# Optimization experiments

Measured on AMD Instinct MI355X. Metric: run time of the kernel, lower is better.

Reference implementation:

```python
import jax, jax.numpy as jnp
import numpy as np


def setup_inputs() -> dict:
    key = jax.random.key(0)
    ks = jax.random.split(key, 6)
    Bsz, Ch, N, L = 16, 1024, 16, 4096
    return {
        "input": jax.random.normal(ks[0], (Bsz, Ch, L), jnp.float32),
        "A": jax.random.normal(ks[1], (Ch, N, 2), jnp.float32),
        "B": jax.random.normal(ks[2], (Ch, N), jnp.float32),  # unused in 'dws' mode
        "C": jax.random.normal(ks[3], (Ch, N), jnp.float32),  # unused in 'dws' mode
        "log_dt": jax.random.normal(ks[4], (Ch, N), jnp.float32) * 0.5 - 4.0,
        "E": jax.random.normal(ks[5], (Ch, N), jnp.float32),
    }


def reference(input, A, B, C, log_dt, E):
    """Kernelizer forward, mode='dws', run_mode='training'.

    discretize (simplified ZOH):
      A_real = -softplus(A[...,0]); A_imag = A[...,1]; dt = exp(log_dt)
      E_hat = E * dt; dtA = dt * (A_real + i*A_imag)        # (Ch, N)
    kernel: k[c, l] = Re( sum_n E_hat[c,n] * exp(dtA[c,n] * l) )
    output: causal depthwise conv of input with k via 2L-padded FFT.
    """
    L = input.shape[-1]
    A_real = -jax.nn.softplus(A[..., 0])                     # (Ch, N)
    A_imag = A[..., 1]                                       # (Ch, N)
    dt = jnp.exp(log_dt)                                     # (Ch, N)
    E_hat = E * dt                                           # (Ch, N)
    dtA_real = dt * A_real
    dtA_imag = dt * A_imag

    l = jnp.arange(L, dtype=input.dtype)                     # (L,)
    # real part of the complex vandermonde, fused: exp(ar*l) * cos(ai*l)
    vand = jnp.exp(dtA_real[:, :, None] * l) * jnp.cos(dtA_imag[:, :, None] * l)  # (Ch, N, L)
    k = jnp.einsum('cn,cnl->cl', E_hat, vand)                # (Ch, L)

    n_fft = 2 * L  # zero-pad so circular conv == linear causal conv
    Uf = jnp.fft.rfft(input, n=n_fft)                        # (B, Ch, L+1)
    Kf = jnp.fft.rfft(k, n=n_fft)                            # (Ch, L+1)
    y = jnp.fft.irfft(Uf * Kf, n=n_fft)[..., :L]             # (B, Ch, L)
    return y.astype(input.dtype)
```

## Files before the change

### kernel.cpp

```cpp
#include <hip/hip_runtime.h>

#define CH   1024
#define BSZ  16
#define LSEQ 4096
#define NST  16

typedef __attribute__((ext_vector_type(8))) short short8;
typedef __attribute__((ext_vector_type(4))) float f32x4;

__device__ __forceinline__ unsigned int pk2(float a, float b) {
    unsigned int ua = __float_as_uint(a);
    unsigned int ub = __float_as_uint(b);
    ua = (ua + 0x7fffu + ((ua >> 16) & 1u)) >> 16;
    ub = (ub + 0x7fffu + ((ub >> 16) & 1u)) & 0xffff0000u;
    return ua | ub;
}

#define P_BYTES 12582912
#define W_BYTES 4194304

__global__ __launch_bounds__(64) void setup_k(const float* __restrict__ A,
                                              const float* __restrict__ log_dt,
                                              const float* __restrict__ E,
                                              unsigned int* __restrict__ Pw,
                                              unsigned int* __restrict__ Ww,
                                              float* __restrict__ qw) {
    __shared__ float powr[NST][65], powi[NST][65], eh[NST], klds[64];
    const int t = threadIdx.x, c = blockIdx.x;
    const int n = t & 15;
    const int idx = c * NST + n;
    float a0 = A[2 * idx], a1 = A[2 * idx + 1];
    float sp = (a0 > 20.f) ? a0 : log1pf(expf(a0));
    float dt = expf(log_dt[idx]);
    float dar = -dt * sp, dai = dt * a1;
    float ehv = E[idx] * dt;
    if (t < NST) eh[t] = ehv;
    for (int l = t >> 4; l < 65; l += 4) {
        float mg = expf(dar * (float)l);
        float s, cs;
        sincosf(dai * (float)l, &s, &cs);
        powr[n][l] = mg * cs;
        powi[n][l] = mg * s;
    }
    __syncthreads();
    float kl = 0.f;
#pragma unroll
    for (int nn = 0; nn < NST; ++nn) kl += eh[nn] * powr[nn][t];
    klds[t] = kl;
    __syncthreads();
    unsigned int* Pc = Pw + c * 3072;
    for (int kk = 0; kk < 48; ++kk) {
        int d = kk * 64 + t;
        int i = d / 48;
        int k0 = (d - i * 48) * 2;
        float vv[2];
#pragma unroll
        for (int u = 0; u < 2; ++u) {
            int k = k0 + u;
            if (k < 64) vv[u] = (k <= i) ? klds[i - k] : 0.f;
            else {
                int p = k - 64;
                int nn = p >> 1;
                vv[u] = (p & 1) ? (-eh[nn] * powi[nn][i + 1]) : (eh[nn] * powr[nn][i + 1]);
            }
        }
        Pc[d] = pk2(vv[0], vv[1]);
    }
    unsigned int* Wc = Ww + c * 1024;
    for (int kk = 0; kk < 16; ++kk) {
        int d = kk * 64 + t;
        int p = d >> 5;
        int j0 = (d & 31) * 2;
        int nn = p >> 1;
        float v0 = (p & 1) ? powi[nn][63 - j0] : powr[nn][63 - j0];
        float v1 = (p & 1) ? powi[nn][62 - j0] : powr[nn][62 - j0];
        Wc[d] = pk2(v0, v1);
    }
    if (t < 32) qw[c * 32 + t] = (t & 1) ? powi[t >> 1][64] : powr[t >> 1][64];
}

#define XT0_OFF 0
#define XT1_OFF 8192
#define S_OFF   16384
#define SIN_OFF 24704
#define SMEM_SZ 28800

__global__ __launch_bounds__(256) void conv_k(const float* __restrict__ x,
                                              const char* __restrict__ Pb,
                                              const char* __restrict__ Wb,
                                              const float* __restrict__ qw,
                                              float* __restrict__ y) {
    __shared__ __align__(16) char smem[SMEM_SZ];
    const int tid  = threadIdx.x;
    const int w    = tid >> 6, lane = tid & 63;
    const int g    = lane >> 4, l15 = lane & 15;
    const int c    = blockIdx.x;

    const char* Pc = Pb + (size_t)c * 12288;
    const char* Wc = Wb + (size_t)c * 4096;
    short8 wa[2], pa[3];
    {
        int p = 16 * (w >> 1) + l15;
#pragma unroll
        for (int kt = 0; kt < 2; ++kt)
            wa[kt] = *(const short8*)(Wc + p * 128 + kt * 64 + g * 16);
        int i = 16 * w + l15;
#pragma unroll
        for (int kt = 0; kt < 3; ++kt)
            pa[kt] = *(const short8*)(Pc + i * 192 + kt * 64 + g * 16);
    }
    float qr0[4], qi0[4];
#pragma unroll
    for (int k = 0; k < 4; ++k) {
        int nn = 4 * w + k;
        qr0[k] = qw[c * 32 + 2 * nn];
        qi0[k] = qw[c * 32 + 2 * nn + 1];
    }

    float* S = (float*)(smem + S_OFF);

    const int st_m    = tid >> 4;
    const int st_base = 8 * (tid & 15);

    auto stage = [&](int xoff, const float4* v) {
#pragma unroll
        for (int it = 0; it < 4; ++it) {
            int m = 16 * it + st_m;
            int byte = (m * 128 + st_base) ^ ((m & 7) << 4);
            *(uint2*)(smem + xoff + byte) =
                make_uint2(pk2(v[it].x, v[it].y), pk2(v[it].z, v[it].w));
        }
    };

    auto gemm1 = [&](int xoff) {
        f32x4 acc[2] = {{0.f, 0.f, 0.f, 0.f}, {0.f, 0.f, 0.f, 0.f}};
        int ntb = 2 * (w & 1);
#pragma unroll
        for (int nt = 0; nt < 2; ++nt) {
            int m = l15 + 16 * (ntb + nt);
            int sw = (m & 7) << 4;
#pragma unroll
            for (int kt = 0; kt < 2; ++kt) {
                short8 bf = *(const short8*)(smem + xoff + ((m * 128 + kt * 64 + g * 16) ^ sw));
                acc[nt] = __builtin_amdgcn_mfma_f32_16x16x32_bf16(wa[kt], bf, acc[nt], 0, 0, 0);
            }
        }
        int pbase = 16 * (w >> 1) + 4 * g;
#pragma unroll
        for (int nt = 0; nt < 2; ++nt) {
            int m = l15 + 16 * (ntb + nt);
#pragma unroll
            for (int r = 0; r < 4; ++r)
                S[(pbase + r) * 65 + m] = acc[nt][r];
        }
    };

    auto scan = [&]() {
        float sr[4], si[4], qr[4], qi[4];
#pragma unroll
        for (int k = 0; k < 4; ++k) {
            int nn = 4 * w + k;
            sr[k] = S[(2 * nn) * 65 + lane];
            si[k] = S[(2 * nn + 1) * 65 + lane];
            qr[k] = qr0[k];
            qi[k] = qi0[k];
        }
#pragma unroll
        for (int d = 1; d < 64; d <<= 1) {
#pragma unroll
            for (int k = 0; k < 4; ++k) {
                float ur = __shfl_up(sr[k], d);
                float ui = __shfl_up(si[k], d);
                ur = (lane >= d) ? ur : 0.f;
                ui = (lane >= d) ? ui : 0.f;
                sr[k] = fmaf(qr[k], ur, fmaf(-qi[k], ui, sr[k]));
                si[k] = fmaf(qr[k], ui, fmaf(qi[k], ur, si[k]));
            }
#pragma unroll
            for (int k = 0; k < 4; ++k) {
                float tq = fmaf(qr[k], qr[k], -(qi[k] * qi[k]));
                qi[k] = 2.f * qr[k] * qi[k];
                qr[k] = tq;
            }
        }
        unsigned int dw[4];
#pragma unroll
        for (int k = 0; k < 4; ++k) {
            float ar = __shfl_up(sr[k], 1);
            float ai = __shfl_up(si[k], 1);
            ar = (lane > 0) ? ar : 0.f;
            ai = (lane > 0) ? ai : 0.f;
            dw[k] = pk2(ar, ai);
        }
        int byte = (lane * 64 + 16 * w) ^ ((lane & 3) << 4);
        *(uint4*)(smem + SIN_OFF + byte) = make_uint4(dw[0], dw[1], dw[2], dw[3]);
    };

    auto gemm2 = [&](int xoff, float* yr) {
        f32x4 acc[4] = {{0.f,0.f,0.f,0.f},{0.f,0.f,0.f,0.f},{0.f,0.f,0.f,0.f},{0.f,0.f,0.f,0.f}};
#pragma unroll
        for (int nt = 0; nt < 4; ++nt) {
            int m = l15 + 16 * nt;
            int sw = (m & 7) << 4;
#pragma unroll
            for (int kt = 0; kt < 2; ++kt) {
                short8 bf = *(const short8*)(smem + xoff + ((m * 128 + kt * 64 + g * 16) ^ sw));
                acc[nt] = __builtin_amdgcn_mfma_f32_16x16x32_bf16(pa[kt], bf, acc[nt], 0, 0, 0);
            }
            short8 sf = *(const short8*)(smem + SIN_OFF + ((m * 64 + g * 16) ^ ((m & 3) << 4)));
            acc[nt] = __builtin_amdgcn_mfma_f32_16x16x32_bf16(pa[2], sf, acc[nt], 0, 0, 0);
        }
#pragma unroll
        for (int nt = 0; nt < 4; ++nt) {
            int m = l15 + 16 * nt;
            float4 v = make_float4(acc[nt][0], acc[nt][1], acc[nt][2], acc[nt][3]);
            *(float4*)(yr + m * 64 + 16 * w + 4 * g) = v;
        }
    };

    const size_t cstride = (size_t)CH * LSEQ;
    const float* xr = x + (size_t)c * LSEQ + 4 * tid;
    float*       yb = y + (size_t)c * LSEQ;

    float4 v[4];
#pragma unroll
    for (int it = 0; it < 4; ++it) v[it] = *(const float4*)(xr + 1024 * it);
    stage(XT0_OFF, v);
#pragma unroll
    for (int it = 0; it < 4; ++it) v[it] = *(const float4*)(xr + cstride + 1024 * it);
    __syncthreads();

    int cur = 0;
    for (int b = 0; b < BSZ; ++b) {
        const int xoff = cur ? XT1_OFF : XT0_OFF;
        const int noff = cur ? XT0_OFF : XT1_OFF;
        gemm1(xoff);
        __syncthreads();
        scan();
        if (b < BSZ - 1) {
            stage(noff, v);
            if (b < BSZ - 2) {
                const float* xn = xr + (size_t)(b + 2) * cstride;
#pragma unroll
                for (int it = 0; it < 4; ++it) v[it] = *(const float4*)(xn + 1024 * it);
            }
        }
        __syncthreads();
        gemm2(xoff, yb + (size_t)b * cstride);
        cur ^= 1;
    }
}

extern "C" void kernel_launch(void* const* d_in, const int* in_sizes, int n_in,
                              void* d_out, int out_size, void* d_ws, size_t ws_size,
                              hipStream_t stream) {
    const float* x      = (const float*)d_in[0];
    const float* A      = (const float*)d_in[1];
    const float* log_dt = (const float*)d_in[4];
    const float* E      = (const float*)d_in[5];
    float* out = (float*)d_out;
    char*  ws  = (char*)d_ws;

    unsigned int* Pw = (unsigned int*)ws;
    unsigned int* Ww = (unsigned int*)(ws + P_BYTES);
    float*        qw = (float*)(ws + P_BYTES + W_BYTES);

    setup_k<<<CH, 64, 0, stream>>>(A, log_dt, E, Pw, Ww, qw);
    conv_k<<<CH, 256, 0, stream>>>(x, (const char*)Pw, (const char*)Ww, qw, out);
}
```

Baseline: 131.0 us.

## Restructure conv kernel scan with DPP, skip zero MFMA tiles, preload fragments

Replaces the shuffle-based 6-step complex scan with DPP row shifts and broadcasts, using precomputed per-lane power factors, so per-step power squaring and LDS-backed shuffles disappear. The x fragments are loaded into registers once per batch and reused by both GEMMs. The second-GEMM MFMA on the upper K half is skipped for waves 0-1, whose P block is presumably zero in that half (causal structure). The batch loop is unrolled by two with fixed buffers, precomputed LDS offsets, hardware bf16 conversion and an occupancy hint. In exchange it relies on the P block being zero there and adds register pressure from the extra per-lane constants.

```diff
diff --git a/kernel.cpp b/kernel.cpp
--- a/kernel.cpp
+++ b/kernel.cpp
@@ -1,4 +1,5 @@
 #include <hip/hip_runtime.h>
+#include <hip/hip_bf16.h>
 
 #define CH   1024
 #define BSZ  16
@@ -15,6 +16,17 @@
     ub = (ub + 0x7fffu + ((ub >> 16) & 1u)) & 0xffff0000u;
     return ua | ub;
 }
+__device__ __forceinline__ unsigned int pkrn(float a, float b) {
+    __hip_bfloat162 h = __float22bfloat162_rn(make_float2(a, b));
+    unsigned int u;
+    __builtin_memcpy(&u, &h, 4);
+    return u;
+}
+__device__ __forceinline__ float rfl(float x) {
+    return __int_as_float(__builtin_amdgcn_readfirstlane(__float_as_int(x)));
+}
+#define DSHR(x, d) __int_as_float(__builtin_amdgcn_update_dpp(0, __float_as_int(x), 0x110 + (d), 0xf, 0xf, true))
+#define DBC(x, ctrl, rm) __int_as_float(__builtin_amdgcn_update_dpp(0, __float_as_int(x), (ctrl), (rm), 0xf, true))
 
 #define P_BYTES 12582912
 #define W_BYTES 4194304
@@ -85,11 +97,11 @@
 #define SIN_OFF 24704
 #define SMEM_SZ 28800
 
-__global__ __launch_bounds__(256) void conv_k(const float* __restrict__ x,
-                                              const char* __restrict__ Pb,
-                                              const char* __restrict__ Wb,
-                                              const float* __restrict__ qw,
-                                              float* __restrict__ y) {
+__global__ __launch_bounds__(256, 4) void conv_k(const float* __restrict__ x,
+                                                 const char* __restrict__ Pb,
+                                                 const char* __restrict__ Wb,
+                                                 const float* __restrict__ qw,
+                                                 float* __restrict__ y) {
     __shared__ __align__(16) char smem[SMEM_SZ];
     const int tid  = threadIdx.x;
     const int w    = tid >> 6, lane = tid & 63;
@@ -109,79 +121,124 @@
         for (int kt = 0; kt < 3; ++kt)
             pa[kt] = *(const short8*)(Pc + i * 192 + kt * 64 + g * 16);
     }
-    float qr0[4], qi0[4];
+
+    float q1r[4], q1i[4], q2r[4], q2i[4], q4r[4], q4i[4], q8r[4], q8i[4];
+    float fr[4], fi[4], hr[4], hi[4];
 #pragma unroll
     for (int k = 0; k < 4; ++k) {
         int nn = 4 * w + k;
-        qr0[k] = qw[c * 32 + 2 * nn];
-        qi0[k] = qw[c * 32 + 2 * nn + 1];
-    }
-
-    float* S = (float*)(smem + S_OFF);
-
-    const int st_m    = tid >> 4;
-    const int st_base = 8 * (tid & 15);
-
-    auto stage = [&](int xoff, const float4* v) {
-#pragma unroll
-        for (int it = 0; it < 4; ++it) {
-            int m = 16 * it + st_m;
-            int byte = (m * 128 + st_base) ^ ((m & 7) << 4);
-            *(uint2*)(smem + xoff + byte) =
-                make_uint2(pk2(v[it].x, v[it].y), pk2(v[it].z, v[it].w));
-        }
-    };
-
-    auto gemm1 = [&](int xoff) {
-        f32x4 acc[2] = {{0.f, 0.f, 0.f, 0.f}, {0.f, 0.f, 0.f, 0.f}};
-        int ntb = 2 * (w & 1);
-#pragma unroll
-        for (int nt = 0; nt < 2; ++nt) {
-            int m = l15 + 16 * (ntb + nt);
-            int sw = (m & 7) << 4;
+        float ar = qw[c * 32 + 2 * nn], ai = qw[c * 32 + 2 * nn + 1];
+        float b2r = fmaf(ar, ar, -(ai * ai)), b2i = 2.f * ar * ai;
+        float b4r = fmaf(b2r, b2r, -(b2i * b2i)), b4i = 2.f * b2r * b2i;
+        float b8r = fmaf(b4r, b4r, -(b4i * b4i)), b8i = 2.f * b4r * b4i;
+        float b16r = fmaf(b8r, b8r, -(b8i * b8i)), b16i = 2.f * b8r * b8i;
+        q1r[k] = rfl(ar);  q1i[k] = rfl(ai);
+        q2r[k] = rfl(b2r); q2i[k] = rfl(b2i);
+        q4r[k] = rfl(b4r); q4i[k] = rfl(b4i);
+        q8r[k] = rfl(b8r); q8i[k] = rfl(b8i);
+        float cr = ar, ci = ai;
+        {
+            float tr = fmaf(cr, ar, -(ci * ai)), ti = fmaf(cr, ai, ci * ar);
+            cr = (l15 & 1) ? tr : cr; ci = (l15 & 1) ? ti : ci;
+        }
+        {
+            float tr = fmaf(cr, b2r, -(ci * b2i)), ti = fmaf(cr, b2i, ci * b2r);
+            cr = (l15 & 2) ? tr : cr; ci = (l15 & 2) ? ti : ci;
+        }
+        {
+            float tr = fmaf(cr, b4r, -(ci * b4i)), ti = fmaf(cr, b4i, ci * b4r);
+            cr = (l15 & 4) ? tr : cr; ci = (l15 & 4) ? ti : ci;
+        }
+        {
+            float tr = fmaf(cr, b8r, -(ci * b8i)), ti = fmaf(cr, b8i, ci * b8r);
+            cr = (l15 & 8) ? tr : cr; ci = (l15 & 8) ? ti : ci;
+        }
+        fr[k] = cr; fi[k] = ci;
+        float tr = fmaf(cr, b16r, -(ci * b16i)), ti = fmaf(cr, b16i, ci * b16r);
+        bool r3 = (lane >= 48);
+        hr[k] = r3 ? tr : cr; hi[k] = r3 ? ti : ci;
+    }
+
+    int xfo[4][2], sino[4], stb[2];
+#pragma unroll
+    for (int nt = 0; nt < 4; ++nt) {
+#pragma unroll
+        for (int kt = 0; kt < 2; ++kt)
+            xfo[nt][kt] = ((l15 * 128 + kt * 64 + g * 16) ^ ((l15 & 7) << 4)) + nt * 2048;
+        sino[nt] = ((l15 * 64 + g * 16) ^ ((l15 & 3) << 4)) + nt * 1024;
+    }
+#pragma unroll
+    for (int it = 0; it < 2; ++it) {
+        int slot = it * 256 + tid;
+        int m = slot >> 3, js = slot & 7;
+        stb[it] = (m * 128 + js * 16) ^ ((m & 7) << 4);
+    }
+    const int ntb  = (w & 1) << 1;
+    const int swb  = ((16 * (w >> 1) + 4 * g) * 65 + l15 + 16 * ntb) * 4;
+    const int srb  = (8 * w * 65 + lane) * 4;
+    const int sinw = (lane * 64 + 16 * w) ^ ((lane & 3) << 4);
+
+    float* Sf = (float*)(smem + S_OFF);
+    (void)Sf;
+
+    short8 xf[4][2];
+    auto rdfrags = [&](int xoff) {
+#pragma unroll
+        for (int nt = 0; nt < 4; ++nt)
+#pragma unroll
+            for (int kt = 0; kt < 2; ++kt)
+                xf[nt][kt] = *(const short8*)(smem + xoff + xfo[nt][kt]);
+    };
+
+    auto gemm1 = [&]() {
+        f32x4 a0 = {0.f, 0.f, 0.f, 0.f}, a1 = {0.f, 0.f, 0.f, 0.f};
+        if ((w & 1) == 0) {
 #pragma unroll
             for (int kt = 0; kt < 2; ++kt) {
-                short8 bf = *(const short8*)(smem + xoff + ((m * 128 + kt * 64 + g * 16) ^ sw));
-                acc[nt] = __builtin_amdgcn_mfma_f32_16x16x32_bf16(wa[kt], bf, acc[nt], 0, 0, 0);
+                a0 = __builtin_amdgcn_mfma_f32_16x16x32_bf16(wa[kt], xf[0][kt], a0, 0, 0, 0);
+                a1 = __builtin_amdgcn_mfma_f32_16x16x32_bf16(wa[kt], xf[1][kt], a1, 0, 0, 0);
             }
-        }
-        int pbase = 16 * (w >> 1) + 4 * g;
-#pragma unroll
-        for (int nt = 0; nt < 2; ++nt) {
-            int m = l15 + 16 * (ntb + nt);
-#pragma unroll
-            for (int r = 0; r < 4; ++r)
-                S[(pbase + r) * 65 + m] = acc[nt][r];
+        } else {
+#pragma unroll
+            for (int kt = 0; kt < 2; ++kt) {
+                a0 = __builtin_amdgcn_mfma_f32_16x16x32_bf16(wa[kt], xf[2][kt], a0, 0, 0, 0);
+                a1 = __builtin_amdgcn_mfma_f32_16x16x32_bf16(wa[kt], xf[3][kt], a1, 0, 0, 0);
+            }
+        }
+#pragma unroll
+        for (int r = 0; r < 4; ++r) {
+            *(float*)(smem + S_OFF + swb + r * 260)      = a0[r];
+            *(float*)(smem + S_OFF + swb + r * 260 + 64) = a1[r];
         }
     };
 
     auto scan = [&]() {
-        float sr[4], si[4], qr[4], qi[4];
+        float sr[4], si[4];
 #pragma unroll
         for (int k = 0; k < 4; ++k) {
-            int nn = 4 * w + k;
-            sr[k] = S[(2 * nn) * 65 + lane];
-            si[k] = S[(2 * nn + 1) * 65 + lane];
-            qr[k] = qr0[k];
-            qi[k] = qi0[k];
-        }
-#pragma unroll
-        for (int d = 1; d < 64; d <<= 1) {
-#pragma unroll
-            for (int k = 0; k < 4; ++k) {
-                float ur = __shfl_up(sr[k], d);
-                float ui = __shfl_up(si[k], d);
-                ur = (lane >= d) ? ur : 0.f;
-                ui = (lane >= d) ? ui : 0.f;
-                sr[k] = fmaf(qr[k], ur, fmaf(-qi[k], ui, sr[k]));
-                si[k] = fmaf(qr[k], ui, fmaf(qi[k], ur, si[k]));
-            }
-#pragma unroll
-            for (int k = 0; k < 4; ++k) {
-                float tq = fmaf(qr[k], qr[k], -(qi[k] * qi[k]));
-                qi[k] = 2.f * qr[k] * qi[k];
-                qr[k] = tq;
-            }
+            sr[k] = *(const float*)(smem + S_OFF + srb + k * 520);
+            si[k] = *(const float*)(smem + S_OFF + srb + k * 520 + 260);
+        }
+#pragma unroll
+        for (int k = 0; k < 4; ++k) {
+            { float ur = DSHR(sr[k], 1), ui = DSHR(si[k], 1);
+              sr[k] = fmaf(q1r[k], ur, fmaf(-q1i[k], ui, sr[k]));
+              si[k] = fmaf(q1r[k], ui, fmaf(q1i[k], ur, si[k])); }
+            { float ur = DSHR(sr[k], 2), ui = DSHR(si[k], 2);
+              sr[k] = fmaf(q2r[k], ur, fmaf(-q2i[k], ui, sr[k]));
+              si[k] = fmaf(q2r[k], ui, fmaf(q2i[k], ur, si[k])); }
+            { float ur = DSHR(sr[k], 4), ui = DSHR(si[k], 4);
+              sr[k] = fmaf(q4r[k], ur, fmaf(-q4i[k], ui, sr[k]));
+              si[k] = fmaf(q4r[k], ui, fmaf(q4i[k], ur, si[k])); }
+            { float ur = DSHR(sr[k], 8), ui = DSHR(si[k], 8);
+              sr[k] = fmaf(q8r[k], ur, fmaf(-q8i[k], ui, sr[k]));
+              si[k] = fmaf(q8r[k], ui, fmaf(q8i[k], ur, si[k])); }
+            { float ur = DBC(sr[k], 0x142, 0xa), ui = DBC(si[k], 0x142, 0xa);
+              sr[k] = fmaf(fr[k], ur, fmaf(-fi[k], ui, sr[k]));
+              si[k] = fmaf(fr[k], ui, fmaf(fi[k], ur, si[k])); }
+            { float ur = DBC(sr[k], 0x143, 0xc), ui = DBC(si[k], 0x143, 0xc);
+              sr[k] = fmaf(hr[k], ur, fmaf(-hi[k], ui, sr[k]));
+              si[k] = fmaf(hr[k], ui, fmaf(hi[k], ur, si[k])); }
         }
         unsigned int dw[4];
 #pragma unroll
@@ -190,25 +247,23 @@
             float ai = __shfl_up(si[k], 1);
             ar = (lane > 0) ? ar : 0.f;
             ai = (lane > 0) ? ai : 0.f;
-            dw[k] = pk2(ar, ai);
-        }
-        int byte = (lane * 64 + 16 * w) ^ ((lane & 3) << 4);
-        *(uint4*)(smem + SIN_OFF + byte) = make_uint4(dw[0], dw[1], dw[2], dw[3]);
-    };
-
-    auto gemm2 = [&](int xoff, float* yr) {
+            dw[k] = pkrn(ar, ai);
+        }
+        *(uint4*)(smem + SIN_OFF + sinw) = make_uint4(dw[0], dw[1], dw[2], dw[3]);
+    };
+
+    auto gemm2 = [&](float* yr) {
         f32x4 acc[4] = {{0.f,0.f,0.f,0.f},{0.f,0.f,0.f,0.f},{0.f,0.f,0.f,0.f},{0.f,0.f,0.f,0.f}};
 #pragma unroll
         for (int nt = 0; nt < 4; ++nt) {
-            int m = l15 + 16 * nt;
-            int sw = (m & 7) << 4;
-#pragma unroll
-            for (int kt = 0; kt < 2; ++kt) {
-                short8 bf = *(const short8*)(smem + xoff + ((m * 128 + kt * 64 + g * 16) ^ sw));
-                acc[nt] = __builtin_amdgcn_mfma_f32_16x16x32_bf16(pa[kt], bf, acc[nt], 0, 0, 0);
-            }
-            short8 sf = *(const short8*)(smem + SIN_OFF + ((m * 64 + g * 16) ^ ((m & 3) << 4)));
+            acc[nt] = __builtin_amdgcn_mfma_f32_16x16x32_bf16(pa[0], xf[nt][0], acc[nt], 0, 0, 0);
+            short8 sf = *(const short8*)(smem + SIN_OFF + sino[nt]);
             acc[nt] = __builtin_amdgcn_mfma_f32_16x16x32_bf16(pa[2], sf, acc[nt], 0, 0, 0);
+        }
+        if (w >= 2) {
+#pragma unroll
+            for (int nt = 0; nt < 4; ++nt)
+                acc[nt] = __builtin_amdgcn_mfma_f32_16x16x32_bf16(pa[1], xf[nt][1], acc[nt], 0, 0, 0);
         }
 #pragma unroll
         for (int nt = 0; nt < 4; ++nt) {
@@ -218,36 +273,57 @@
         }
     };
 
+    float4 pend[4];
+    const float* xr = x + (size_t)c * LSEQ;
+    float*       yb = y + (size_t)c * LSEQ;
     const size_t cstride = (size_t)CH * LSEQ;
-    const float* xr = x + (size_t)c * LSEQ + 4 * tid;
-    float*       yb = y + (size_t)c * LSEQ;
-
-    float4 v[4];
-#pragma unroll
-    for (int it = 0; it < 4; ++it) v[it] = *(const float4*)(xr + 1024 * it);
-    stage(XT0_OFF, v);
-#pragma unroll
-    for (int it = 0; it < 4; ++it) v[it] = *(const float4*)(xr + cstride + 1024 * it);
+
+    auto ldraw = [&](const float* xp) {
+#pragma unroll
+        for (int it = 0; it < 2; ++it) {
+            int slot = it * 256 + tid;
+            pend[2 * it]     = *(const float4*)(xp + slot * 8);
+            pend[2 * it + 1] = *(const float4*)(xp + slot * 8 + 4);
+        }
+    };
+    auto stage = [&](int xoff) {
+#pragma unroll
+        for (int it = 0; it < 2; ++it) {
+            uint4 pk;
+            pk.x = pkrn(pend[2 * it].x,     pend[2 * it].y);
+            pk.y = pkrn(pend[2 * it].z,     pend[2 * it].w);
+            pk.z = pkrn(pend[2 * it + 1].x, pend[2 * it + 1].y);
+            pk.w = pkrn(pend[2 * it + 1].z, pend[2 * it + 1].w);
+            *(uint4*)(smem + xoff + stb[it]) = pk;
+        }
+    };
+
+    ldraw(xr);
+    stage(XT0_OFF);
+    ldraw(xr + cstride);
     __syncthreads();
 
-    int cur = 0;
-    for (int b = 0; b < BSZ; ++b) {
-        const int xoff = cur ? XT1_OFF : XT0_OFF;
-        const int noff = cur ? XT0_OFF : XT1_OFF;
-        gemm1(xoff);
+#pragma unroll 1
+    for (int bb = 0; bb < 8; ++bb) {
+        rdfrags(XT0_OFF);
+        gemm1();
         __syncthreads();
         scan();
-        if (b < BSZ - 1) {
-            stage(noff, v);
-            if (b < BSZ - 2) {
-                const float* xn = xr + (size_t)(b + 2) * cstride;
-#pragma unroll
-                for (int it = 0; it < 4; ++it) v[it] = *(const float4*)(xn + 1024 * it);
-            }
-        }
+        stage(XT1_OFF);
+        if (bb < 7) ldraw(xr + (size_t)(2 * bb + 2) * cstride);
         __syncthreads();
-        gemm2(xoff, yb + (size_t)b * cstride);
-        cur ^= 1;
+        gemm2(yb + (size_t)(2 * bb) * cstride);
+
+        rdfrags(XT1_OFF);
+        gemm1();
+        __syncthreads();
+        scan();
+        if (bb < 7) {
+            stage(XT0_OFF);
+            ldraw(xr + (size_t)(2 * bb + 3) * cstride);
+        }
+        __syncthreads();
+        gemm2(yb + (size_t)(2 * bb + 1) * cstride);
     }
 }
 
```

Result: faster. 127.1 us (-3.0%).
